# Kernel tuning notes

Hardware: AMD Instinct MI355X
Metric: run time of the kernel (lower is better)

Reference implementation:

```python
import jax, jax.numpy as jnp
import numpy as np
import math

DIMS, HEAD = 1024, 16
HD = DIMS // HEAD          # 64
B, CTX = 4, 1024
MAX_ITER, THRESH = 3, 0.5  # temp=1.0 -> q temperature scaling branch is skipped (as in torch)
LOG10_21 = math.log10(1.0 + 4000.0 / 200.0)


def _freq_angles(c):
    # compute_freqs_base: 0.2*(10**linspace(0, log10(21), d/2) - 1), custom_freqs = 36000/220 * base
    d2 = HD // 2
    mel = 10.0 ** jnp.linspace(0.0, LOG10_21, d2) - 1.0
    freqs = (36000.0 / 220.0) * (200.0 * mel / 1000.0)        # [d2]
    t = jnp.arange(c, dtype=jnp.float32)
    return t[:, None] * freqs[None, :]                          # [c, d2]


def _rope(x, ang):
    # lucidrains rotary_embedding_torch convention: interleaved pairs (x0,x1),(x2,x3),...
    x1, x2 = x[..., 0::2], x[..., 1::2]
    cos, sin = jnp.cos(ang), jnp.sin(ang)
    out = jnp.stack([x1 * cos - x2 * sin, x1 * sin + x2 * cos], axis=-1)
    return out.reshape(x.shape)


def _rms(x, w):
    eps = jnp.finfo(x.dtype).eps  # torch nn.RMSNorm eps=None default
    return x * jax.lax.rsqrt(jnp.mean(jnp.square(x), -1, keepdims=True) + eps) * w


def _sdpa(q, k, v):
    # mask is always None in this module's forward -> non-causal SDPA
    s = jnp.einsum('bhqd,bhkd->bhqk', q, k) / math.sqrt(q.shape[-1])
    return jnp.einsum('bhqk,bhkd->bhqd', jax.nn.softmax(s, -1), v)


def _focus(x, xa, P):
    # x: [b, cq, D] queries, xa: [b, ck, D] keys/values. In our configs cq == ck == eff_span.
    b, cq, D = x.shape
    ck = xa.shape[1]
    q = _rms(x, P['wq_norm']) @ P['Wq'] + P['bq']
    q = q.reshape(b, cq, HEAD, HD).transpose(0, 2, 1, 3)                 # b h c d
    kv = _rms(xa, P['wkv_norm']) @ P['Wkv'] + P['bkv']
    kv = kv.reshape(b, ck, 2, HEAD, HD).transpose(2, 0, 3, 1, 4)         # kv b h c d
    k, v = kv[0], kv[1]
    q = _rope(q, _freq_angles(cq))
    k = _rope(k, _freq_angles(ck))

    e = min(cq, ck)  # static; equals cq in all call sites here
    curq, kc, vc = q, k[:, :, :e], v[:, :, :e]
    prev = jnp.zeros_like(q)
    attn_out = jnp.zeros_like(q)
    done = jnp.asarray(False)
    for it in range(MAX_ITER):
        # torch: q/k/v re-projected from current state EVERY iteration (k,v compound)
        qp = curq[:, :, :e] @ P['Wlq'] + P['blq']
        kp = kc @ P['Wlk'] + P['blk']
        vp = vc @ P['Wlv'] + P['blv']
        attn = _sdpa(_rms(qp, P['wln']), _rms(kp, P['wln']), vp)         # == iter_out since e == cq
        diff = jnp.mean(jnp.abs(attn - prev))
        stop = (diff < THRESH) & (it > 0) & (~done)
        attn_out = jnp.where(done, attn_out, attn)  # on the break iteration attn_out = iter_out
        done = done | stop
        curq = jnp.where(done, curq, curq + attn)
        prev = jnp.where(done, prev, attn)
        kc = jnp.where(done, kc, kp)
        vc = jnp.where(done, vc, vp)
    return attn_out.transpose(0, 2, 1, 3).reshape(b, cq, D)             # b c (h d)


def _slide(x, P):
    # win_size = head_dim; only the first win_size keys of each span are ever used
    b, ctx, D = x.shape
    w = HD
    off = w // HEAD                       # span_len - win_size
    nwin = ctx // w                       # ctx chosen as a multiple of w
    starts = jnp.maximum(jnp.arange(nwin) * w - off, 0)
    kidx = starts[:, None] + jnp.arange(w)[None, :]                      # [nwin, w]
    qwin = x.reshape(b, nwin, w, D).transpose(1, 0, 2, 3)                # [nwin, b, w, D]
    kwin = x[:, kidx, :].transpose(1, 0, 2, 3)                           # [nwin, b, w, D]
    outw = jax.vmap(lambda xq, xk: _focus(xq, xk, P))(qwin, kwin)
    return outw.transpose(1, 0, 2, 3).reshape(b, ctx, D)


def _forward(x, xa, P):
    xw = _slide(x, P)
    xaw = _slide(xa, P)
    out = _focus(xw, xaw, P)
    return out @ P['Wo'] + P['bo']        # Dropout(0.01) is identity in eval


def setup_inputs() -> dict:
    key = jax.random.key(0)
    ks = jax.random.split(key, 8)
    s = 0.02
    f32 = jnp.float32
    return {
        'x': jax.random.normal(ks[0], (B, CTX, DIMS), f32),
        'xa': jax.random.normal(ks[1], (B, CTX, DIMS), f32),
        'wq_norm': jnp.ones((DIMS,), f32),
        'Wq': jax.random.normal(ks[2], (DIMS, DIMS), f32) * s,
        'bq': jnp.zeros((DIMS,), f32),
        'wkv_norm': jnp.ones((DIMS,), f32),
        'Wkv': jax.random.normal(ks[3], (DIMS, 2 * DIMS), f32) * s,
        'bkv': jnp.zeros((2 * DIMS,), f32),
        'wln': jnp.ones((HD,), f32),
        'Wlq': jax.random.normal(ks[4], (HD, HD), f32) * s,
        'blq': jnp.zeros((HD,), f32),
        'Wlk': jax.random.normal(ks[5], (HD, HD), f32) * s,
        'blk': jnp.zeros((HD,), f32),
        'Wlv': jax.random.normal(ks[6], (HD, HD), f32) * s,
        'blv': jnp.zeros((HD,), f32),
        'Wo': jax.random.normal(ks[7], (DIMS, DIMS), f32) * s,
        'bo': jnp.zeros((DIMS,), f32),
    }


def reference(x, xa, wq_norm, Wq, bq, wkv_norm, Wkv, bkv, wln, Wlq, blq, Wlk, blk, Wlv, blv, Wo, bo):
    P = dict(wq_norm=wq_norm, Wq=Wq, bq=bq, wkv_norm=wkv_norm, Wkv=Wkv, bkv=bkv, wln=wln,
             Wlq=Wlq, blq=blq, Wlk=Wlk, blk=blk, Wlv=Wlv, blv=blv, Wo=Wo, bo=bo)
    return _forward(x, xa, P)
```

## Files before the change

### kernel.cpp

```cpp
#include <hip/hip_runtime.h>
#include <math.h>

#define TPB 256

static __device__ __forceinline__ float4 mk4(float a, float b, float c, float d) {
  float4 r; r.x = a; r.y = b; r.z = c; r.w = d; return r;
}

__global__ __launch_bounds__(TPB) void k_tables(float* __restrict__ cosb,
                                                float* __restrict__ sinb) {
  int gid = blockIdx.x * TPB + threadIdx.x;
  if (gid >= 1024 * 32) return;
  int t = gid >> 5, j = gid & 31;
  const double Ld = 1.3222192947339193;
  float Lf = (float)Ld;
  float mlog;
  if (j == 31) {
    mlog = Lf;
  } else {
    float stepf = (float)((double)j / 31.0);
    mlog = (float)((double)Lf * (double)stepf);
  }
  float p = (float)pow(10.0, (double)mlog);
  float mel = p - 1.0f;
  float t2 = (200.0f * mel) / 1000.0f;
  float freq = 163.63636363636363f * t2;
  float ang = (float)t * freq;
  double a = (double)ang;
  cosb[gid] = (float)cos(a);
  sinb[gid] = (float)sin(a);
}

__global__ __launch_bounds__(TPB) void k_rowinv(const float* __restrict__ X,
                                                float* __restrict__ inv) {
  __shared__ float red[4];
  int row = blockIdx.x;
  int tid = threadIdx.x;
  float4 v = *(const float4*)(X + (size_t)row * 1024 + tid * 4);
  float ss = v.x * v.x + v.y * v.y + v.z * v.z + v.w * v.w;
#pragma unroll
  for (int m = 1; m < 64; m <<= 1) ss += __shfl_xor(ss, m);
  if ((tid & 63) == 0) red[tid >> 6] = ss;
  __syncthreads();
  if (tid == 0) {
    float s = ((red[0] + red[1]) + (red[2] + red[3]));
    float mm = s * (1.0f / 1024.0f) + 1.1920928955078125e-7f;
    inv[row] = (float)(1.0 / sqrt((double)mm));
  }
}

__global__ __launch_bounds__(TPB) void k_gemm128(
    const float* __restrict__ X, const float* __restrict__ inv,
    const float* __restrict__ wn, const float* __restrict__ W,
    const float* __restrict__ bias, float* __restrict__ o0,
    float* __restrict__ o1, int N, int mode) {
  __shared__ float As[16][132];
  __shared__ float Bs[16][132];
  int tid = threadIdx.x;
  int bx = blockIdx.x, by = blockIdx.y;
  int tx = tid & 15, ty = tid >> 4;
  float c[8][8];
#pragma unroll
  for (int i = 0; i < 8; ++i)
#pragma unroll
    for (int j = 0; j < 8; ++j) c[i][j] = 0.0f;

  int arow = tid >> 1;
  float sA = 1.0f;
  if (inv) sA = inv[by * 128 + arow];
  const float* Xrow = X + (size_t)(by * 128 + arow) * 1024;

  for (int k0 = 0; k0 < 1024; k0 += 16) {
#pragma unroll
    for (int u = 0; u < 2; ++u) {
      int kq = ((tid & 1) * 2 + u) * 4;
      float4 a4 = *(const float4*)(Xrow + k0 + kq);
      if (wn) {
        float4 w4 = *(const float4*)(wn + k0 + kq);
        a4.x *= w4.x; a4.y *= w4.y; a4.z *= w4.z; a4.w *= w4.w;
      }
      a4.x *= sA; a4.y *= sA; a4.z *= sA; a4.w *= sA;
      As[kq + 0][arow] = a4.x;
      As[kq + 1][arow] = a4.y;
      As[kq + 2][arow] = a4.z;
      As[kq + 3][arow] = a4.w;
    }
#pragma unroll
    for (int u = 0; u < 2; ++u) {
      int kr = tid >> 4;
      int c4 = ((tid & 15) * 2 + u) * 4;
      *(float4*)&Bs[kr][c4] =
          *(const float4*)(W + (size_t)(k0 + kr) * N + bx * 128 + c4);
    }
    __syncthreads();
#pragma unroll
    for (int kk = 0; kk < 16; ++kk) {
      float4 a0 = *(const float4*)&As[kk][ty * 4];
      float4 a1 = *(const float4*)&As[kk][64 + ty * 4];
      float4 b0 = *(const float4*)&Bs[kk][tx * 4];
      float4 b1 = *(const float4*)&Bs[kk][64 + tx * 4];
      float av[8] = {a0.x, a0.y, a0.z, a0.w, a1.x, a1.y, a1.z, a1.w};
      float bv[8] = {b0.x, b0.y, b0.z, b0.w, b1.x, b1.y, b1.z, b1.w};
#pragma unroll
      for (int i = 0; i < 8; ++i)
#pragma unroll
        for (int j = 0; j < 8; ++j) c[i][j] += av[i] * bv[j];
    }
    __syncthreads();
  }

#pragma unroll
  for (int jh = 0; jh < 2; ++jh) {
    int colbase = bx * 128 + jh * 64 + tx * 4;
    float4 bb = {0.f, 0.f, 0.f, 0.f};
    if (bias) bb = *(const float4*)(bias + colbase);
#pragma unroll
    for (int ih = 0; ih < 2; ++ih) {
#pragma unroll
      for (int i2 = 0; i2 < 4; ++i2) {
        int row = by * 128 + ih * 64 + ty * 4 + i2;
        int ci = ih * 4 + i2;
        float4 o;
        o.x = c[ci][jh * 4 + 0] + bb.x;
        o.y = c[ci][jh * 4 + 1] + bb.y;
        o.z = c[ci][jh * 4 + 2] + bb.z;
        o.w = c[ci][jh * 4 + 3] + bb.w;
        if (mode == 0) {
          *(float4*)(o0 + (size_t)row * N + colbase) = o;
        } else {
          int b = row >> 10, t = row & 1023;
          float* dst = o0;
          int cc = colbase;
          if (mode == 2 && colbase >= 1024) { dst = o1; cc = colbase - 1024; }
          int ch = cc >> 6, d = cc & 63;
          *(float4*)(dst + ((size_t)((b * 16 + ch) * 1024 + t)) * 64 + d) = o;
        }
      }
    }
  }
}

__global__ __launch_bounds__(TPB) void k_rope(float* __restrict__ A, int mask,
                                              const float* __restrict__ cosb,
                                              const float* __restrict__ sinb) {
  int gid = blockIdx.x * TPB + threadIdx.x;
  int j = gid & 31;
  int row = gid >> 5;
  int t = row & 1023;
  int aidx = ((t & mask) << 5) + j;
  float cc = cosb[aidx], sn = sinb[aidx];
  size_t base = (size_t)row * 64;
  float x1 = A[base + 2 * j], x2 = A[base + 2 * j + 1];
  A[base + 2 * j] = x1 * cc - x2 * sn;
  A[base + 2 * j + 1] = x1 * sn + x2 * cc;
}

__global__ __launch_bounds__(TPB) void k_gather(
    const float* __restrict__ K, const float* __restrict__ V,
    float* __restrict__ kc, float* __restrict__ vc,
    const float* __restrict__ cosb, const float* __restrict__ sinb) {
  int gid = blockIdx.x * TPB + threadIdx.x;
  int j = gid & 31;
  int tl = (gid >> 5) & 63;
  int win = (gid >> 11) & 15;
  int h = (gid >> 15) & 15;
  int b = gid >> 19;
  int sw = win * 64 - 4;
  if (win == 0) sw = 0;
  size_t bh = (size_t)(b * 16 + h) * 1024;
  size_t src = (bh + sw + tl) * 64;
  size_t dst = (bh + win * 64 + tl) * 64;
  int aidx = (tl << 5) + j;
  float cc = cosb[aidx], sn = sinb[aidx];
  float k1 = K[src + 2 * j], k2 = K[src + 2 * j + 1];
  kc[dst + 2 * j] = k1 * cc - k2 * sn;
  kc[dst + 2 * j + 1] = k1 * sn + k2 * cc;
  vc[dst + 2 * j] = V[src + 2 * j];
  vc[dst + 2 * j + 1] = V[src + 2 * j + 1];
}

__global__ __launch_bounds__(TPB) void k_proj(
    const float* __restrict__ curq, float* __restrict__ kc,
    float* __restrict__ vc, float* __restrict__ qph, float* __restrict__ kph,
    const float* __restrict__ Wlq, const float* __restrict__ blq,
    const float* __restrict__ Wlk, const float* __restrict__ blk,
    const float* __restrict__ Wlv, const float* __restrict__ blv,
    const float* __restrict__ wln, int CQ, const int* __restrict__ flags) {
  int RT = CQ >> 4;
  int bid = blockIdx.x;
  int rt = bid % RT;
  int rest = bid / RT;
  int h = rest & 15; rest >>= 4;
  int b = rest & 3;
  int win = rest >> 2;
  if (flags && flags[win]) return;
  __shared__ float qs[16][68], ksm[16][68], vsm[16][68];
  __shared__ float Wqs[4096], Wks[4096], Wvs[4096];
  int tid = threadIdx.x;
#pragma unroll
  for (int i = 0; i < 4; ++i) {
    int f4 = (i * 256 + tid) * 4;
    *(float4*)&Wqs[f4] = *(const float4*)(Wlq + f4);
    *(float4*)&Wks[f4] = *(const float4*)(Wlk + f4);
    *(float4*)&Wvs[f4] = *(const float4*)(Wlv + f4);
  }
  int lr = tid >> 4, c4 = (tid & 15) * 4;
  int bh = b * 16 + h;
  size_t rowbase = (size_t)bh * 1024 + (size_t)win * CQ + rt * 16;
  size_t g = (rowbase + lr) * 64 + c4;
  *(float4*)&qs[lr][c4] = *(const float4*)(curq + g);
  *(float4*)&ksm[lr][c4] = *(const float4*)(kc + g);
  *(float4*)&vsm[lr][c4] = *(const float4*)(vc + g);
  __syncthreads();
  int r = tid >> 4, cg = tid & 15;
  const float eps = 1.1920928955078125e-7f;
  float4 wl4 = *(const float4*)(wln + cg * 4);
  size_t orow = (rowbase + r) * 64 + cg * 4;
  float4 acc;
  float ssum, rms;
  acc = *(const float4*)(blq + cg * 4);
#pragma unroll 8
  for (int k = 0; k < 64; ++k) {
    float xv = qs[r][k];
    float4 w4 = *(const float4*)&Wqs[k * 64 + cg * 4];
    acc.x += xv * w4.x; acc.y += xv * w4.y;
    acc.z += xv * w4.z; acc.w += xv * w4.w;
  }
  ssum = acc.x * acc.x + acc.y * acc.y + acc.z * acc.z + acc.w * acc.w;
#pragma unroll
  for (int m = 1; m < 16; m <<= 1) ssum += __shfl_xor(ssum, m);
  rms = (float)(1.0 / sqrt((double)(ssum * 0.015625f + eps)));
  {
    float4 o;
    o.x = acc.x * rms * wl4.x; o.y = acc.y * rms * wl4.y;
    o.z = acc.z * rms * wl4.z; o.w = acc.w * rms * wl4.w;
    *(float4*)(qph + orow) = o;
  }
  acc = *(const float4*)(blk + cg * 4);
#pragma unroll 8
  for (int k = 0; k < 64; ++k) {
    float xv = ksm[r][k];
    float4 w4 = *(const float4*)&Wks[k * 64 + cg * 4];
    acc.x += xv * w4.x; acc.y += xv * w4.y;
    acc.z += xv * w4.z; acc.w += xv * w4.w;
  }
  *(float4*)(kc + orow) = acc;
  ssum = acc.x * acc.x + acc.y * acc.y + acc.z * acc.z + acc.w * acc.w;
#pragma unroll
  for (int m = 1; m < 16; m <<= 1) ssum += __shfl_xor(ssum, m);
  rms = (float)(1.0 / sqrt((double)(ssum * 0.015625f + eps)));
  {
    float4 o;
    o.x = acc.x * rms * wl4.x; o.y = acc.y * rms * wl4.y;
    o.z = acc.z * rms * wl4.z; o.w = acc.w * rms * wl4.w;
    *(float4*)(kph + orow) = o;
  }
  acc = *(const float4*)(blv + cg * 4);
#pragma unroll 8
  for (int k = 0; k < 64; ++k) {
    float xv = vsm[r][k];
    float4 w4 = *(const float4*)&Wvs[k * 64 + cg * 4];
    acc.x += xv * w4.x; acc.y += xv * w4.y;
    acc.z += xv * w4.z; acc.w += xv * w4.w;
  }
  *(float4*)(vc + orow) = acc;
}

template <int FRAG>
__global__ __launch_bounds__(TPB) void k_attn2(
    const float* __restrict__ qph, const float* __restrict__ kph,
    const float* __restrict__ vbuf, float* __restrict__ curq,
    float* __restrict__ prevb, float* __restrict__ outb,
    float* __restrict__ diffp, const int* __restrict__ flags, int NQT,
    int nt, int mode) {
  constexpr int QT = FRAG * 16;
  constexpr int RS = (FRAG == 8) ? 3 : 2;
  int bid = blockIdx.x;
  int qt = bid % NQT;
  int bh = bid / NQT;
  int h = bh & 15, b = bh >> 4;
  if (mode == 2 && flags[(nt == 1) ? qt : 0]) return;
  __shared__ float sQP[QT * 64];
  __shared__ float sK[64 * 64];
  __shared__ float sV[64 * 64];
  int tid = threadIdx.x;
  int tx = tid & 15, ty = tid >> 4;
  size_t bh1024 = (size_t)bh * 1024;
  int q0 = qt * QT;
  int qb[FRAG], kb[4];
#pragma unroll
  for (int i = 0; i < FRAG; ++i) qb[i] = (ty * FRAG + i) << 6;
#pragma unroll
  for (int j = 0; j < 4; ++j) kb[j] = (tx * 4 + j) << 6;

  float m[FRAG], l[FRAG], acc[FRAG][4];
#pragma unroll
  for (int i = 0; i < FRAG; ++i) {
    m[i] = -INFINITY; l[i] = 0.0f;
    acc[i][0] = acc[i][1] = acc[i][2] = acc[i][3] = 0.0f;
  }
  int kstart = (nt == 1) ? q0 : 0;
  const float SCL = 0.18033688011112042f;

  for (int kt = 0; kt < nt; ++kt) {
    int k0 = kstart + kt * 64;
#pragma unroll
    for (int u = 0; u < FRAG; ++u) {
      int f4 = u * 256 + tid;
      int row = f4 >> 4, ch = f4 & 15;
      int cp = ((ch ^ (row >> RS)) & 15) << 2;
      *(float4*)&sQP[(row << 6) + cp] =
          *(const float4*)(qph + (bh1024 + q0 + row) * 64 + (ch << 2));
    }
#pragma unroll
    for (int u = 0; u < 4; ++u) {
      int f4 = u * 256 + tid;
      int row = f4 >> 4, ch = f4 & 15;
      int cp = ((ch ^ (row >> 2)) & 15) << 2;
      *(float4*)&sK[(row << 6) + cp] =
          *(const float4*)(kph + (bh1024 + k0 + row) * 64 + (ch << 2));
      *(float4*)&sV[(row << 6) + cp] =
          *(const float4*)(vbuf + (bh1024 + k0 + row) * 64 + (ch << 2));
    }
    __syncthreads();

    float s[FRAG][4];
#pragma unroll
    for (int i = 0; i < FRAG; ++i)
      s[i][0] = s[i][1] = s[i][2] = s[i][3] = 0.0f;
#pragma unroll 2
    for (int d4 = 0; d4 < 16; ++d4) {
      int kcp = ((d4 ^ tx) & 15) << 2;
      float4 k4[4];
#pragma unroll
      for (int j = 0; j < 4; ++j) k4[j] = *(const float4*)&sK[kb[j] + kcp];
      int qcp = ((d4 ^ ty) & 15) << 2;
#pragma unroll
      for (int i = 0; i < FRAG; ++i) {
        float4 q4 = *(const float4*)&sQP[qb[i] + qcp];
#pragma unroll
        for (int j = 0; j < 4; ++j) {
          s[i][j] += q4.x * k4[j].x;
          s[i][j] += q4.y * k4[j].y;
          s[i][j] += q4.z * k4[j].z;
          s[i][j] += q4.w * k4[j].w;
        }
      }
    }
#pragma unroll
    for (int i = 0; i < FRAG; ++i) {
      s[i][0] *= SCL; s[i][1] *= SCL; s[i][2] *= SCL; s[i][3] *= SCL;
      float r0 = fmaxf(fmaxf(s[i][0], s[i][1]), fmaxf(s[i][2], s[i][3]));
#pragma unroll
      for (int mm = 1; mm < 16; mm <<= 1) r0 = fmaxf(r0, __shfl_xor(r0, mm));
      float mnew = fmaxf(m[i], r0);
      float sc = exp2f(m[i] - mnew);
      float rs = 0.0f;
#pragma unroll
      for (int j = 0; j < 4; ++j) {
        float pv = exp2f(s[i][j] - mnew);
        s[i][j] = pv;
        rs += pv;
      }
#pragma unroll
      for (int mm = 1; mm < 16; mm <<= 1) rs += __shfl_xor(rs, mm);
      l[i] = l[i] * sc + rs;
      m[i] = mnew;
      acc[i][0] *= sc; acc[i][1] *= sc; acc[i][2] *= sc; acc[i][3] *= sc;
    }
    {
      int pcw = ((tx ^ ty) & 15) << 2;
#pragma unroll
      for (int i = 0; i < FRAG; ++i)
        *(float4*)&sQP[qb[i] + pcw] = mk4(s[i][0], s[i][1], s[i][2], s[i][3]);
    }
#pragma unroll 2
    for (int k4 = 0; k4 < 16; ++k4) {
      int vcp = ((k4 ^ tx) & 15) << 2;
      float4 v4[4];
#pragma unroll
      for (int kk = 0; kk < 4; ++kk)
        v4[kk] = *(const float4*)&sV[((k4 * 4 + kk) << 6) + vcp];
      int pcp = ((k4 ^ ty) & 15) << 2;
#pragma unroll
      for (int i = 0; i < FRAG; ++i) {
        float4 p4 = *(const float4*)&sQP[qb[i] + pcp];
        acc[i][0] += p4.x * v4[0].x; acc[i][1] += p4.x * v4[0].y;
        acc[i][2] += p4.x * v4[0].z; acc[i][3] += p4.x * v4[0].w;
        acc[i][0] += p4.y * v4[1].x; acc[i][1] += p4.y * v4[1].y;
        acc[i][2] += p4.y * v4[1].z; acc[i][3] += p4.y * v4[1].w;
        acc[i][0] += p4.z * v4[2].x; acc[i][1] += p4.z * v4[2].y;
        acc[i][2] += p4.z * v4[2].z; acc[i][3] += p4.z * v4[2].w;
        acc[i][0] += p4.w * v4[3].x; acc[i][1] += p4.w * v4[3].y;
        acc[i][2] += p4.w * v4[3].z; acc[i][3] += p4.w * v4[3].w;
      }
    }
    __syncthreads();
  }
  float ds = 0.0f;
#pragma unroll
  for (int i = 0; i < FRAG; ++i) {
    int t = q0 + ty * FRAG + i;
    float4 att;
    att.x = acc[i][0] / l[i];
    att.y = acc[i][1] / l[i];
    att.z = acc[i][2] / l[i];
    att.w = acc[i][3] / l[i];
    size_t base = (bh1024 + t) * 64 + tx * 4;
    size_t obase = ((size_t)b * 1024 + t) * 1024 + h * 64 + tx * 4;
    if (mode == 0) {
      *(float4*)(prevb + base) = att;
      float4 cq = *(const float4*)(curq + base);
      cq.x += att.x; cq.y += att.y; cq.z += att.z; cq.w += att.w;
      *(float4*)(curq + base) = cq;
    } else if (mode == 1) {
      float4 pv = *(const float4*)(prevb + base);
      ds += fabsf(att.x - pv.x) + fabsf(att.y - pv.y) +
            fabsf(att.z - pv.z) + fabsf(att.w - pv.w);
      float4 cq = *(const float4*)(curq + base);
      cq.x += att.x; cq.y += att.y; cq.z += att.z; cq.w += att.w;
      *(float4*)(curq + base) = cq;
      *(float4*)(outb + obase) = att;
    } else {
      *(float4*)(outb + obase) = att;
    }
  }
  if (mode == 1) {
    float* red = sK;
    red[tid] = ds;
    __syncthreads();
    for (int s2 = 128; s2 > 0; s2 >>= 1) {
      if (tid < s2) red[tid] += red[tid + s2];
      __syncthreads();
    }
    if (tid == 0) diffp[bid] = red[0];
  }
}

__global__ __launch_bounds__(64) void k_finalize(const float* __restrict__ diffp,
                                                 int* __restrict__ flags,
                                                 int nwin, int nper,
                                                 float count) {
  int w = threadIdx.x;
  if (w < nwin) {
    float s = 0.0f;
    for (int i = 0; i < nper; ++i) s += diffp[w + i * nwin];
    flags[w] = (s / count < 0.5f) ? 1 : 0;
  }
}

extern "C" void kernel_launch(void* const* d_in, const int* in_sizes, int n_in,
                              void* d_out, int out_size, void* d_ws,
                              size_t ws_size, hipStream_t stream) {
  const float* x = (const float*)d_in[0];
  const float* xa = (const float*)d_in[1];
  const float* wqn = (const float*)d_in[2];
  const float* Wq = (const float*)d_in[3];
  const float* bq = (const float*)d_in[4];
  const float* wkvn = (const float*)d_in[5];
  const float* Wkv = (const float*)d_in[6];
  const float* bkv = (const float*)d_in[7];
  const float* wln = (const float*)d_in[8];
  const float* Wlq = (const float*)d_in[9];
  const float* blq = (const float*)d_in[10];
  const float* Wlk = (const float*)d_in[11];
  const float* blk = (const float*)d_in[12];
  const float* Wlv = (const float*)d_in[13];
  const float* blv = (const float*)d_in[14];
  const float* Wo = (const float*)d_in[15];
  const float* bo = (const float*)d_in[16];

  float* ws = (float*)d_ws;
  const size_t SLOT = (size_t)4 * 16 * 1024 * 64;
  float* xw = ws;
  float* xaw = ws + SLOT;
  float* Q = ws + 2 * SLOT;
  float* K = ws + 3 * SLOT;
  float* V = ws + 4 * SLOT;
  float* kc = ws + 5 * SLOT;
  float* vc = ws + 6 * SLOT;
  float* prev = ws + 7 * SLOT;
  float* qph = ws + 8 * SLOT;
  float* kph = ws + 9 * SLOT;
  float* misc = ws + 10 * SLOT;
  float* inv = misc;
  float* cosb = misc + 8192;
  float* sinb = cosb + 32768;
  float* diffp = sinb + 32768;
  int* flags = (int*)(diffp + 4096);

  k_tables<<<128, TPB, 0, stream>>>(cosb, sinb);

  for (int sl = 0; sl < 2; ++sl) {
    const float* Xin = sl ? xa : x;
    float* Xout = sl ? xaw : xw;
    k_rowinv<<<4096, TPB, 0, stream>>>(Xin, inv);
    k_gemm128<<<dim3(8, 32), TPB, 0, stream>>>(Xin, inv, wqn, Wq, bq, Q, nullptr, 1024, 1);
    k_gemm128<<<dim3(16, 32), TPB, 0, stream>>>(Xin, inv, wkvn, Wkv, bkv, K, V, 2048, 2);
    k_rope<<<8192, TPB, 0, stream>>>(Q, 63, cosb, sinb);
    k_gather<<<8192, TPB, 0, stream>>>(K, V, kc, vc, cosb, sinb);
    k_proj<<<4096, TPB, 0, stream>>>(Q, kc, vc, qph, kph, Wlq, blq, Wlk, blk, Wlv, blv, wln, 64, nullptr);
    k_attn2<4><<<1024, TPB, 0, stream>>>(qph, kph, vc, Q, prev, Xout, diffp, nullptr, 16, 1, 0);
    k_proj<<<4096, TPB, 0, stream>>>(Q, kc, vc, qph, kph, Wlq, blq, Wlk, blk, Wlv, blv, wln, 64, nullptr);
    k_attn2<4><<<1024, TPB, 0, stream>>>(qph, kph, vc, Q, prev, Xout, diffp, nullptr, 16, 1, 1);
    k_finalize<<<1, 64, 0, stream>>>(diffp, flags, 16, 64, 262144.0f);
    k_proj<<<4096, TPB, 0, stream>>>(Q, kc, vc, qph, kph, Wlq, blq, Wlk, blk, Wlv, blv, wln, 64, flags);
    k_attn2<4><<<1024, TPB, 0, stream>>>(qph, kph, vc, Q, prev, Xout, diffp, flags, 16, 1, 2);
  }

  k_rowinv<<<4096, TPB, 0, stream>>>(xw, inv);
  k_gemm128<<<dim3(8, 32), TPB, 0, stream>>>(xw, inv, wqn, Wq, bq, Q, nullptr, 1024, 1);
  k_rowinv<<<4096, TPB, 0, stream>>>(xaw, inv);
  k_gemm128<<<dim3(16, 32), TPB, 0, stream>>>(xaw, inv, wkvn, Wkv, bkv, K, V, 2048, 2);
  k_rope<<<8192, TPB, 0, stream>>>(Q, 1023, cosb, sinb);
  k_rope<<<8192, TPB, 0, stream>>>(K, 1023, cosb, sinb);
  float* fout = xw;
  k_proj<<<4096, TPB, 0, stream>>>(Q, K, V, qph, kph, Wlq, blq, Wlk, blk, Wlv, blv, wln, 1024, nullptr);
  k_attn2<8><<<512, TPB, 0, stream>>>(qph, kph, V, Q, prev, fout, diffp, nullptr, 8, 16, 0);
  k_proj<<<4096, TPB, 0, stream>>>(Q, K, V, qph, kph, Wlq, blq, Wlk, blk, Wlv, blv, wln, 1024, nullptr);
  k_attn2<8><<<512, TPB, 0, stream>>>(qph, kph, V, Q, prev, fout, diffp, nullptr, 8, 16, 1);
  k_finalize<<<1, 64, 0, stream>>>(diffp, flags, 1, 512, 4194304.0f);
  k_proj<<<4096, TPB, 0, stream>>>(Q, K, V, qph, kph, Wlq, blq, Wlk, blk, Wlv, blv, wln, 1024, flags);
  k_attn2<8><<<512, TPB, 0, stream>>>(qph, kph, V, Q, prev, fout, diffp, flags, 8, 16, 2);

  k_gemm128<<<dim3(8, 32), TPB, 0, stream>>>(fout, nullptr, nullptr, Wo, bo, (float*)d_out, nullptr, 1024, 0);
}
```

Before: 2.657 ms.

## Fuse sliding-window rope, projections and attention iterations into one kernel; widen full attention tiles

The windowed phase used separate rope, gather, projection and attention kernels for each iteration. These become a single k_slide kernel that keeps each 64-row window in shared memory across the first two iterations, which removes the intermediate global traffic and most launches. The full-context attention kernel is also rewritten to use 128-key tiles with 8x8 register blocking. This cuts the number of tile loads and syncs, at the cost of more registers and 96KB of shared memory, which limits occupancy to one block per CU.

Result: faster. 2.493 ms (-6.2%).

```diff
diff --git a/kernel.cpp b/kernel.cpp
--- a/kernel.cpp
+++ b/kernel.cpp
@@ -5,6 +5,13 @@
 
 static __device__ __forceinline__ float4 mk4(float a, float b, float c, float d) {
   float4 r; r.x = a; r.y = b; r.z = c; r.w = d; return r;
+}
+
+static __device__ __forceinline__ float4 ld4s(const float* buf, int row, int ch) {
+  return *(const float4*)&buf[(row << 6) + (((ch ^ (row >> 2)) & 15) << 2)];
+}
+static __device__ __forceinline__ void st4s(float* buf, int row, int ch, float4 v) {
+  *(float4*)&buf[(row << 6) + (((ch ^ (row >> 2)) & 15) << 2)] = v;
 }
 
 __global__ __launch_bounds__(TPB) void k_tables(float* __restrict__ cosb,
@@ -153,30 +160,6 @@
   float x1 = A[base + 2 * j], x2 = A[base + 2 * j + 1];
   A[base + 2 * j] = x1 * cc - x2 * sn;
   A[base + 2 * j + 1] = x1 * sn + x2 * cc;
-}
-
-__global__ __launch_bounds__(TPB) void k_gather(
-    const float* __restrict__ K, const float* __restrict__ V,
-    float* __restrict__ kc, float* __restrict__ vc,
-    const float* __restrict__ cosb, const float* __restrict__ sinb) {
-  int gid = blockIdx.x * TPB + threadIdx.x;
-  int j = gid & 31;
-  int tl = (gid >> 5) & 63;
-  int win = (gid >> 11) & 15;
-  int h = (gid >> 15) & 15;
-  int b = gid >> 19;
-  int sw = win * 64 - 4;
-  if (win == 0) sw = 0;
-  size_t bh = (size_t)(b * 16 + h) * 1024;
-  size_t src = (bh + sw + tl) * 64;
-  size_t dst = (bh + win * 64 + tl) * 64;
-  int aidx = (tl << 5) + j;
-  float cc = cosb[aidx], sn = sinb[aidx];
-  float k1 = K[src + 2 * j], k2 = K[src + 2 * j + 1];
-  kc[dst + 2 * j] = k1 * cc - k2 * sn;
-  kc[dst + 2 * j + 1] = k1 * sn + k2 * cc;
-  vc[dst + 2 * j] = V[src + 2 * j];
-  vc[dst + 2 * j + 1] = V[src + 2 * j + 1];
 }
 
 __global__ __launch_bounds__(TPB) void k_proj(
@@ -266,98 +249,306 @@
   *(float4*)(vc + orow) = acc;
 }
 
-template <int FRAG>
-__global__ __launch_bounds__(TPB) void k_attn2(
+static __device__ __forceinline__ void slide_proj_one(
+    float* src, float* rawdst, float* ndst, const float* __restrict__ W,
+    const float* __restrict__ bias, float4 wl4, int tx, int ty) {
+  const float eps = 1.1920928955078125e-7f;
+  float4 bb = *(const float4*)(bias + tx * 4);
+  float4 acc[4];
+#pragma unroll
+  for (int i = 0; i < 4; ++i) acc[i] = bb;
+#pragma unroll 2
+  for (int k4 = 0; k4 < 16; ++k4) {
+    const float* w = W + (k4 * 4) * 64 + tx * 4;
+    float4 w0 = *(const float4*)(w);
+    float4 w1 = *(const float4*)(w + 64);
+    float4 w2 = *(const float4*)(w + 128);
+    float4 w3 = *(const float4*)(w + 192);
+#pragma unroll
+    for (int i = 0; i < 4; ++i) {
+      float4 a4 = ld4s(src, ty * 4 + i, k4);
+      acc[i].x += a4.x * w0.x; acc[i].y += a4.x * w0.y;
+      acc[i].z += a4.x * w0.z; acc[i].w += a4.x * w0.w;
+      acc[i].x += a4.y * w1.x; acc[i].y += a4.y * w1.y;
+      acc[i].z += a4.y * w1.z; acc[i].w += a4.y * w1.w;
+      acc[i].x += a4.z * w2.x; acc[i].y += a4.z * w2.y;
+      acc[i].z += a4.z * w2.z; acc[i].w += a4.z * w2.w;
+      acc[i].x += a4.w * w3.x; acc[i].y += a4.w * w3.y;
+      acc[i].z += a4.w * w3.z; acc[i].w += a4.w * w3.w;
+    }
+  }
+#pragma unroll
+  for (int i = 0; i < 4; ++i) {
+    int row = ty * 4 + i;
+    if (rawdst) st4s(rawdst, row, tx, acc[i]);
+    if (ndst) {
+      float ssum = acc[i].x * acc[i].x + acc[i].y * acc[i].y +
+                   acc[i].z * acc[i].z + acc[i].w * acc[i].w;
+#pragma unroll
+      for (int mm = 1; mm < 16; mm <<= 1) ssum += __shfl_xor(ssum, mm);
+      float rms = (float)(1.0 / sqrt((double)(ssum * 0.015625f + eps)));
+      st4s(ndst, row, tx, mk4(acc[i].x * rms * wl4.x, acc[i].y * rms * wl4.y,
+                              acc[i].z * rms * wl4.z, acc[i].w * rms * wl4.w));
+    }
+  }
+}
+
+__global__ __launch_bounds__(TPB) void k_slide(
+    const float* __restrict__ Qg, const float* __restrict__ Kg,
+    const float* __restrict__ Vg, float* __restrict__ curqg,
+    float* __restrict__ kcg, float* __restrict__ vcg, float* __restrict__ outb,
+    float* __restrict__ diffp, const int* __restrict__ flags,
+    const float* __restrict__ cosb, const float* __restrict__ sinb,
+    const float* __restrict__ Wlq, const float* __restrict__ blq,
+    const float* __restrict__ Wlk, const float* __restrict__ blk,
+    const float* __restrict__ Wlv, const float* __restrict__ blv,
+    const float* __restrict__ wln, int mode) {
+  int bid = blockIdx.x;
+  int win = bid & 15, bh = bid >> 4;
+  int h = bh & 15, b = bh >> 4;
+  if (mode == 2 && flags[win]) return;
+  __shared__ float sX[4096], sKc[4096], sVc[4096], sQp[4096], sKp[4096];
+  int tid = threadIdx.x;
+  int tx = tid & 15, ty = tid >> 4;
+  size_t bh1024 = (size_t)bh * 1024;
+  int t0 = win * 64;
+  const float SCL = 0.18033688011112042f;
+
+  if (mode == 0) {
+    int sw = (win == 0) ? 0 : win * 64 - 4;
+#pragma unroll
+    for (int u = 0; u < 4; ++u) {
+      int f4 = u * 256 + tid;
+      int row = f4 >> 4, ch = f4 & 15;
+      int aidx = (row << 5) + ch * 2;
+      float c0 = cosb[aidx], s0 = sinb[aidx];
+      float c1 = cosb[aidx + 1], s1 = sinb[aidx + 1];
+      float4 q = *(const float4*)(Qg + (bh1024 + t0 + row) * 64 + ch * 4);
+      st4s(sX, row, ch, mk4(q.x * c0 - q.y * s0, q.x * s0 + q.y * c0,
+                            q.z * c1 - q.w * s1, q.z * s1 + q.w * c1));
+      float4 k = *(const float4*)(Kg + (bh1024 + sw + row) * 64 + ch * 4);
+      st4s(sKc, row, ch, mk4(k.x * c0 - k.y * s0, k.x * s0 + k.y * c0,
+                             k.z * c1 - k.w * s1, k.z * s1 + k.w * c1));
+      st4s(sVc, row, ch,
+           *(const float4*)(Vg + (bh1024 + sw + row) * 64 + ch * 4));
+    }
+  } else {
+#pragma unroll
+    for (int u = 0; u < 4; ++u) {
+      int f4 = u * 256 + tid;
+      int row = f4 >> 4, ch = f4 & 15;
+      size_t g = (bh1024 + t0 + row) * 64 + ch * 4;
+      st4s(sX, row, ch, *(const float4*)(curqg + g));
+      st4s(sKc, row, ch, *(const float4*)(kcg + g));
+      st4s(sVc, row, ch, *(const float4*)(vcg + g));
+    }
+  }
+  float4 wl4 = *(const float4*)(wln + tx * 4);
+  float4 prev4[4];
+  int niter = (mode == 0) ? 2 : 1;
+  for (int it = 0; it < niter; ++it) {
+    __syncthreads();
+    slide_proj_one(sX, nullptr, sQp, Wlq, blq, wl4, tx, ty);
+    slide_proj_one(sKc, sKc, sKp, Wlk, blk, wl4, tx, ty);
+    slide_proj_one(sVc, sVc, nullptr, Wlv, blv, wl4, tx, ty);
+    __syncthreads();
+    float s4[4][4];
+#pragma unroll
+    for (int i = 0; i < 4; ++i)
+      s4[i][0] = s4[i][1] = s4[i][2] = s4[i][3] = 0.0f;
+#pragma unroll 4
+    for (int d4 = 0; d4 < 16; ++d4) {
+      float4 kv[4];
+#pragma unroll
+      for (int j = 0; j < 4; ++j) kv[j] = ld4s(sKp, tx * 4 + j, d4);
+#pragma unroll
+      for (int i = 0; i < 4; ++i) {
+        float4 q4 = ld4s(sQp, ty * 4 + i, d4);
+#pragma unroll
+        for (int j = 0; j < 4; ++j) {
+          s4[i][j] += q4.x * kv[j].x;
+          s4[i][j] += q4.y * kv[j].y;
+          s4[i][j] += q4.z * kv[j].z;
+          s4[i][j] += q4.w * kv[j].w;
+        }
+      }
+    }
+    float lrow[4];
+#pragma unroll
+    for (int i = 0; i < 4; ++i) {
+      s4[i][0] *= SCL; s4[i][1] *= SCL; s4[i][2] *= SCL; s4[i][3] *= SCL;
+      float r0 = fmaxf(fmaxf(s4[i][0], s4[i][1]), fmaxf(s4[i][2], s4[i][3]));
+#pragma unroll
+      for (int mm = 1; mm < 16; mm <<= 1) r0 = fmaxf(r0, __shfl_xor(r0, mm));
+      float rs = 0.0f;
+#pragma unroll
+      for (int j = 0; j < 4; ++j) {
+        float pv = exp2f(s4[i][j] - r0);
+        s4[i][j] = pv;
+        rs += pv;
+      }
+#pragma unroll
+      for (int mm = 1; mm < 16; mm <<= 1) rs += __shfl_xor(rs, mm);
+      lrow[i] = rs;
+    }
+#pragma unroll
+    for (int i = 0; i < 4; ++i)
+      st4s(sQp, ty * 4 + i, tx, mk4(s4[i][0], s4[i][1], s4[i][2], s4[i][3]));
+    float4 av[4];
+#pragma unroll
+    for (int i = 0; i < 4; ++i) av[i] = mk4(0.f, 0.f, 0.f, 0.f);
+#pragma unroll 4
+    for (int k4 = 0; k4 < 16; ++k4) {
+      float4 v4[4];
+#pragma unroll
+      for (int kk = 0; kk < 4; ++kk) v4[kk] = ld4s(sVc, k4 * 4 + kk, tx);
+#pragma unroll
+      for (int i = 0; i < 4; ++i) {
+        float4 p4 = ld4s(sQp, ty * 4 + i, k4);
+        av[i].x += p4.x * v4[0].x; av[i].y += p4.x * v4[0].y;
+        av[i].z += p4.x * v4[0].z; av[i].w += p4.x * v4[0].w;
+        av[i].x += p4.y * v4[1].x; av[i].y += p4.y * v4[1].y;
+        av[i].z += p4.y * v4[1].z; av[i].w += p4.y * v4[1].w;
+        av[i].x += p4.z * v4[2].x; av[i].y += p4.z * v4[2].y;
+        av[i].z += p4.z * v4[2].z; av[i].w += p4.z * v4[2].w;
+        av[i].x += p4.w * v4[3].x; av[i].y += p4.w * v4[3].y;
+        av[i].z += p4.w * v4[3].z; av[i].w += p4.w * v4[3].w;
+      }
+    }
+#pragma unroll
+    for (int i = 0; i < 4; ++i) {
+      av[i].x /= lrow[i]; av[i].y /= lrow[i];
+      av[i].z /= lrow[i]; av[i].w /= lrow[i];
+    }
+    if (mode == 0 && it == 0) {
+#pragma unroll
+      for (int i = 0; i < 4; ++i) {
+        prev4[i] = av[i];
+        int row = ty * 4 + i;
+        float4 cq = ld4s(sX, row, tx);
+        cq.x += av[i].x; cq.y += av[i].y; cq.z += av[i].z; cq.w += av[i].w;
+        st4s(sX, row, tx, cq);
+      }
+    } else if (mode == 0) {
+      float ds = 0.0f;
+#pragma unroll
+      for (int i = 0; i < 4; ++i) {
+        int row = ty * 4 + i;
+        ds += fabsf(av[i].x - prev4[i].x) + fabsf(av[i].y - prev4[i].y) +
+              fabsf(av[i].z - prev4[i].z) + fabsf(av[i].w - prev4[i].w);
+        float4 cq = ld4s(sX, row, tx);
+        cq.x += av[i].x; cq.y += av[i].y; cq.z += av[i].z; cq.w += av[i].w;
+        st4s(sX, row, tx, cq);
+        size_t g = (bh1024 + t0 + row) * 64 + tx * 4;
+        *(float4*)(curqg + g) = cq;
+        *(float4*)(kcg + g) = ld4s(sKc, row, tx);
+        *(float4*)(vcg + g) = ld4s(sVc, row, tx);
+        size_t obase = ((size_t)b * 1024 + t0 + row) * 1024 + h * 64 + tx * 4;
+        *(float4*)(outb + obase) = av[i];
+      }
+      __syncthreads();
+      float* red = sKp;
+      red[tid] = ds;
+      __syncthreads();
+      for (int s2 = 128; s2 > 0; s2 >>= 1) {
+        if (tid < s2) red[tid] += red[tid + s2];
+        __syncthreads();
+      }
+      if (tid == 0) diffp[bid] = red[0];
+    } else {
+#pragma unroll
+      for (int i = 0; i < 4; ++i) {
+        int row = ty * 4 + i;
+        size_t obase = ((size_t)b * 1024 + t0 + row) * 1024 + h * 64 + tx * 4;
+        *(float4*)(outb + obase) = av[i];
+      }
+    }
+  }
+}
+
+__global__ __launch_bounds__(TPB, 1) void k_attn3(
     const float* __restrict__ qph, const float* __restrict__ kph,
     const float* __restrict__ vbuf, float* __restrict__ curq,
     float* __restrict__ prevb, float* __restrict__ outb,
-    float* __restrict__ diffp, const int* __restrict__ flags, int NQT,
-    int nt, int mode) {
-  constexpr int QT = FRAG * 16;
-  constexpr int RS = (FRAG == 8) ? 3 : 2;
+    float* __restrict__ diffp, const int* __restrict__ flags, int NQT, int nt,
+    int mode) {
   int bid = blockIdx.x;
   int qt = bid % NQT;
   int bh = bid / NQT;
   int h = bh & 15, b = bh >> 4;
-  if (mode == 2 && flags[(nt == 1) ? qt : 0]) return;
-  __shared__ float sQP[QT * 64];
-  __shared__ float sK[64 * 64];
-  __shared__ float sV[64 * 64];
+  if (mode == 2 && flags[0]) return;
+  __shared__ float region[24576];
+  float* sQ = region;
+  float* sK = region + 8192;
+  float* sP = region;
+  float* sV = region + 16384;
   int tid = threadIdx.x;
   int tx = tid & 15, ty = tid >> 4;
   size_t bh1024 = (size_t)bh * 1024;
-  int q0 = qt * QT;
-  int qb[FRAG], kb[4];
-#pragma unroll
-  for (int i = 0; i < FRAG; ++i) qb[i] = (ty * FRAG + i) << 6;
-#pragma unroll
-  for (int j = 0; j < 4; ++j) kb[j] = (tx * 4 + j) << 6;
-
-  float m[FRAG], l[FRAG], acc[FRAG][4];
-#pragma unroll
-  for (int i = 0; i < FRAG; ++i) {
+  int q0 = qt * 128;
+
+  float m[8], l[8], acc[8][4];
+#pragma unroll
+  for (int i = 0; i < 8; ++i) {
     m[i] = -INFINITY; l[i] = 0.0f;
     acc[i][0] = acc[i][1] = acc[i][2] = acc[i][3] = 0.0f;
   }
-  int kstart = (nt == 1) ? q0 : 0;
   const float SCL = 0.18033688011112042f;
 
   for (int kt = 0; kt < nt; ++kt) {
-    int k0 = kstart + kt * 64;
-#pragma unroll
-    for (int u = 0; u < FRAG; ++u) {
+    int k0 = kt * 128;
+#pragma unroll
+    for (int u = 0; u < 8; ++u) {
       int f4 = u * 256 + tid;
       int row = f4 >> 4, ch = f4 & 15;
-      int cp = ((ch ^ (row >> RS)) & 15) << 2;
-      *(float4*)&sQP[(row << 6) + cp] =
-          *(const float4*)(qph + (bh1024 + q0 + row) * 64 + (ch << 2));
-    }
-#pragma unroll
-    for (int u = 0; u < 4; ++u) {
-      int f4 = u * 256 + tid;
-      int row = f4 >> 4, ch = f4 & 15;
-      int cp = ((ch ^ (row >> 2)) & 15) << 2;
+      int cp = ((ch ^ (row >> 3)) & 15) << 2;
+      *(float4*)&sQ[(row << 6) + cp] =
+          *(const float4*)(qph + (bh1024 + q0 + row) * 64 + ch * 4);
       *(float4*)&sK[(row << 6) + cp] =
-          *(const float4*)(kph + (bh1024 + k0 + row) * 64 + (ch << 2));
+          *(const float4*)(kph + (bh1024 + k0 + row) * 64 + ch * 4);
       *(float4*)&sV[(row << 6) + cp] =
-          *(const float4*)(vbuf + (bh1024 + k0 + row) * 64 + (ch << 2));
-    }
-    __syncthreads();
-
-    float s[FRAG][4];
-#pragma unroll
-    for (int i = 0; i < FRAG; ++i)
-      s[i][0] = s[i][1] = s[i][2] = s[i][3] = 0.0f;
+          *(const float4*)(vbuf + (bh1024 + k0 + row) * 64 + ch * 4);
+    }
+    __syncthreads();
+    float s[8][8];
+#pragma unroll
+    for (int i = 0; i < 8; ++i)
+#pragma unroll
+      for (int j = 0; j < 8; ++j) s[i][j] = 0.0f;
 #pragma unroll 2
     for (int d4 = 0; d4 < 16; ++d4) {
-      int kcp = ((d4 ^ tx) & 15) << 2;
-      float4 k4[4];
-#pragma unroll
-      for (int j = 0; j < 4; ++j) k4[j] = *(const float4*)&sK[kb[j] + kcp];
-      int qcp = ((d4 ^ ty) & 15) << 2;
-#pragma unroll
-      for (int i = 0; i < FRAG; ++i) {
-        float4 q4 = *(const float4*)&sQP[qb[i] + qcp];
-#pragma unroll
-        for (int j = 0; j < 4; ++j) {
-          s[i][j] += q4.x * k4[j].x;
-          s[i][j] += q4.y * k4[j].y;
-          s[i][j] += q4.z * k4[j].z;
-          s[i][j] += q4.w * k4[j].w;
+      float4 kv[8];
+#pragma unroll
+      for (int j = 0; j < 8; ++j)
+        kv[j] = *(const float4*)&sK[((tx * 8 + j) << 6) +
+                                    (((d4 ^ tx) & 15) << 2)];
+#pragma unroll
+      for (int i = 0; i < 8; ++i) {
+        float4 q4 = *(const float4*)&sQ[((ty * 8 + i) << 6) +
+                                        (((d4 ^ ty) & 15) << 2)];
+#pragma unroll
+        for (int j = 0; j < 8; ++j) {
+          s[i][j] += q4.x * kv[j].x;
+          s[i][j] += q4.y * kv[j].y;
+          s[i][j] += q4.z * kv[j].z;
+          s[i][j] += q4.w * kv[j].w;
         }
       }
     }
 #pragma unroll
-    for (int i = 0; i < FRAG; ++i) {
-      s[i][0] *= SCL; s[i][1] *= SCL; s[i][2] *= SCL; s[i][3] *= SCL;
-      float r0 = fmaxf(fmaxf(s[i][0], s[i][1]), fmaxf(s[i][2], s[i][3]));
+    for (int i = 0; i < 8; ++i) {
+#pragma unroll
+      for (int j = 0; j < 8; ++j) s[i][j] *= SCL;
+      float r0 = s[i][0];
+#pragma unroll
+      for (int j = 1; j < 8; ++j) r0 = fmaxf(r0, s[i][j]);
 #pragma unroll
       for (int mm = 1; mm < 16; mm <<= 1) r0 = fmaxf(r0, __shfl_xor(r0, mm));
       float mnew = fmaxf(m[i], r0);
       float sc = exp2f(m[i] - mnew);
       float rs = 0.0f;
 #pragma unroll
-      for (int j = 0; j < 4; ++j) {
+      for (int j = 0; j < 8; ++j) {
         float pv = exp2f(s[i][j] - mnew);
         s[i][j] = pv;
         rs += pv;
@@ -368,23 +559,28 @@
       m[i] = mnew;
       acc[i][0] *= sc; acc[i][1] *= sc; acc[i][2] *= sc; acc[i][3] *= sc;
     }
-    {
-      int pcw = ((tx ^ ty) & 15) << 2;
-#pragma unroll
-      for (int i = 0; i < FRAG; ++i)
-        *(float4*)&sQP[qb[i] + pcw] = mk4(s[i][0], s[i][1], s[i][2], s[i][3]);
+    __syncthreads();
+#pragma unroll
+    for (int i = 0; i < 8; ++i) {
+      int q = ty * 8 + i;
+      *(float4*)&sP[(q << 7) + ((((2 * tx) ^ ty) & 31) << 2)] =
+          mk4(s[i][0], s[i][1], s[i][2], s[i][3]);
+      *(float4*)&sP[(q << 7) + ((((2 * tx + 1) ^ ty) & 31) << 2)] =
+          mk4(s[i][4], s[i][5], s[i][6], s[i][7]);
     }
 #pragma unroll 2
-    for (int k4 = 0; k4 < 16; ++k4) {
-      int vcp = ((k4 ^ tx) & 15) << 2;
+    for (int k4 = 0; k4 < 32; ++k4) {
       float4 v4[4];
 #pragma unroll
-      for (int kk = 0; kk < 4; ++kk)
-        v4[kk] = *(const float4*)&sV[((k4 * 4 + kk) << 6) + vcp];
-      int pcp = ((k4 ^ ty) & 15) << 2;
-#pragma unroll
-      for (int i = 0; i < FRAG; ++i) {
-        float4 p4 = *(const float4*)&sQP[qb[i] + pcp];
+      for (int kk = 0; kk < 4; ++kk) {
+        int row = k4 * 4 + kk;
+        v4[kk] =
+            *(const float4*)&sV[(row << 6) + (((tx ^ (row >> 3)) & 15) << 2)];
+      }
+#pragma unroll
+      for (int i = 0; i < 8; ++i) {
+        float4 p4 = *(const float4*)&sP[((ty * 8 + i) << 7) +
+                                        (((k4 ^ ty) & 31) << 2)];
         acc[i][0] += p4.x * v4[0].x; acc[i][1] += p4.x * v4[0].y;
         acc[i][2] += p4.x * v4[0].z; acc[i][3] += p4.x * v4[0].w;
         acc[i][0] += p4.y * v4[1].x; acc[i][1] += p4.y * v4[1].y;
@@ -399,8 +595,8 @@
   }
   float ds = 0.0f;
 #pragma unroll
-  for (int i = 0; i < FRAG; ++i) {
-    int t = q0 + ty * FRAG + i;
+  for (int i = 0; i < 8; ++i) {
+    int t = q0 + ty * 8 + i;
     float4 att;
     att.x = acc[i][0] / l[i];
     att.y = acc[i][1] / l[i];
@@ -426,7 +622,8 @@
     }
   }
   if (mode == 1) {
-    float* red = sK;
+    __syncthreads();
+    float* red = region;
     red[tid] = ds;
     __syncthreads();
     for (int s2 = 128; s2 > 0; s2 >>= 1) {
@@ -497,15 +694,13 @@
     k_rowinv<<<4096, TPB, 0, stream>>>(Xin, inv);
     k_gemm128<<<dim3(8, 32), TPB, 0, stream>>>(Xin, inv, wqn, Wq, bq, Q, nullptr, 1024, 1);
     k_gemm128<<<dim3(16, 32), TPB, 0, stream>>>(Xin, inv, wkvn, Wkv, bkv, K, V, 2048, 2);
-    k_rope<<<8192, TPB, 0, stream>>>(Q, 63, cosb, sinb);
-    k_gather<<<8192, TPB, 0, stream>>>(K, V, kc, vc, cosb, sinb);
-    k_proj<<<4096, TPB, 0, stream>>>(Q, kc, vc, qph, kph, Wlq, blq, Wlk, blk, Wlv, blv, wln, 64, nullptr);
-    k_attn2<4><<<1024, TPB, 0, stream>>>(qph, kph, vc, Q, prev, Xout, diffp, nullptr, 16, 1, 0);
-    k_proj<<<4096, TPB, 0, stream>>>(Q, kc, vc, qph, kph, Wlq, blq, Wlk, blk, Wlv, blv, wln, 64, nullptr);
-    k_attn2<4><<<1024, TPB, 0, stream>>>(qph, kph, vc, Q, prev, Xout, diffp, nullptr, 16, 1, 1);
+    k_slide<<<1024, TPB, 0, stream>>>(Q, K, V, Q, kc, vc, Xout, diffp, nullptr,
+                                      cosb, sinb, Wlq, blq, Wlk, blk, Wlv, blv,
+                                      wln, 0);
     k_finalize<<<1, 64, 0, stream>>>(diffp, flags, 16, 64, 262144.0f);
-    k_proj<<<4096, TPB, 0, stream>>>(Q, kc, vc, qph, kph, Wlq, blq, Wlk, blk, Wlv, blv, wln, 64, flags);
-    k_attn2<4><<<1024, TPB, 0, stream>>>(qph, kph, vc, Q, prev, Xout, diffp, flags, 16, 1, 2);
+    k_slide<<<1024, TPB, 0, stream>>>(Q, K, V, Q, kc, vc, Xout, diffp, flags,
+                                      cosb, sinb, Wlq, blq, Wlk, blk, Wlv, blv,
+                                      wln, 2);
   }
 
   k_rowinv<<<4096, TPB, 0, stream>>>(xw, inv);
@@ -516,12 +711,12 @@
   k_rope<<<8192, TPB, 0, stream>>>(K, 1023, cosb, sinb);
   float* fout = xw;
   k_proj<<<4096, TPB, 0, stream>>>(Q, K, V, qph, kph, Wlq, blq, Wlk, blk, Wlv, blv, wln, 1024, nullptr);
-  k_attn2<8><<<512, TPB, 0, stream>>>(qph, kph, V, Q, prev, fout, diffp, nullptr, 8, 16, 0);
+  k_attn3<<<512, TPB, 0, stream>>>(qph, kph, V, Q, prev, fout, diffp, nullptr, 8, 8, 0);
   k_proj<<<4096, TPB, 0, stream>>>(Q, K, V, qph, kph, Wlq, blq, Wlk, blk, Wlv, blv, wln, 1024, nullptr);
-  k_attn2<8><<<512, TPB, 0, stream>>>(qph, kph, V, Q, prev, fout, diffp, nullptr, 8, 16, 1);
+  k_attn3<<<512, TPB, 0, stream>>>(qph, kph, V, Q, prev, fout, diffp, nullptr, 8, 8, 1);
   k_finalize<<<1, 64, 0, stream>>>(diffp, flags, 1, 512, 4194304.0f);
   k_proj<<<4096, TPB, 0, stream>>>(Q, K, V, qph, kph, Wlq, blq, Wlk, blk, Wlv, blv, wln, 1024, flags);
-  k_attn2<8><<<512, TPB, 0, stream>>>(qph, kph, V, Q, prev, fout, diffp, flags, 8, 16, 2);
+  k_attn3<<<512, TPB, 0, stream>>>(qph, kph, V, Q, prev, fout, diffp, flags, 8, 8, 2);
 
   k_gemm128<<<dim3(8, 32), TPB, 0, stream>>>(fout, nullptr, nullptr, Wo, bo, (float*)d_out, nullptr, 1024, 0);
 }
```
